# Kernel optimization log

Measured on AMD Instinct MI355X. Metric: run time of the kernel, lower is better.

## Reference

```python
import jax, jax.numpy as jnp
import numpy as np

D_MODEL = 2048
N_HEAD = 16
B, T = 2, 2048
D_HEAD = D_MODEL // N_HEAD          # 128
D_Q = D_MODEL // 3                  # 682
D_KV = D_MODEL // 2                 # 1024
D_QK_N = D_HEAD // 2                # 64
D_QK_R = D_HEAD // 2                # 64
LN_EPS = 1e-5


def setup_inputs() -> dict:
    key = jax.random.key(0)
    ks = jax.random.split(key, 8)
    s = 0.02
    return {
        'x': jax.random.normal(ks[0], (B, T, D_MODEL), dtype=jnp.float32),
        'Wdq_w': jax.random.normal(ks[1], (D_Q, D_MODEL), dtype=jnp.float32) * s,
        'Wdq_b': jnp.zeros((D_Q,), jnp.float32),
        'qn_g': jnp.ones((D_Q,), jnp.float32),
        'qn_b': jnp.zeros((D_Q,), jnp.float32),
        'Wuq_w': jax.random.normal(ks[2], (D_MODEL, D_Q), dtype=jnp.float32) * s,
        'Wuq_b': jnp.zeros((D_MODEL,), jnp.float32),
        'Wdkv_w': jax.random.normal(ks[3], (D_KV + D_QK_R, D_MODEL), dtype=jnp.float32) * s,
        'Wdkv_b': jnp.zeros((D_KV + D_QK_R,), jnp.float32),
        'kvn_g': jnp.ones((D_KV,), jnp.float32),
        'kvn_b': jnp.zeros((D_KV,), jnp.float32),
        'Wukv_w': jax.random.normal(ks[4], (D_MODEL + N_HEAD * D_QK_N, D_KV), dtype=jnp.float32) * s,
        'Wukv_b': jnp.zeros((D_MODEL + N_HEAD * D_QK_N,), jnp.float32),
        'Wo_w': jax.random.normal(ks[5], (D_MODEL, D_MODEL), dtype=jnp.float32) * s,
        'Wo_b': jnp.zeros((D_MODEL,), jnp.float32),
    }


def _linear(x, w, b):
    return jnp.einsum('...i,oi->...o', x, w) + b


def _layernorm(x, g, b):
    mu = jnp.mean(x, axis=-1, keepdims=True)
    var = jnp.mean(jnp.square(x - mu), axis=-1, keepdims=True)
    return (x - mu) * jax.lax.rsqrt(var + LN_EPS) * g + b


def _rotary(x):
    # Faithful to source: positions are taken from axis 1 of x (B, A, T, d)
    A, d = x.shape[1], x.shape[-1]
    inv_freq = (1.0 / 10000.0) ** (jnp.arange(0, d, 2, dtype=jnp.float32) / d)
    freqs = jnp.arange(A, dtype=jnp.float32)[:, None] * inv_freq[None, :]
    cos = jnp.cos(freqs)[None, :, None, :]
    sin = jnp.sin(freqs)[None, :, None, :]
    x1, x2 = jnp.split(x, 2, axis=-1)
    return jnp.concatenate([x1 * cos + x2 * sin, -x1 * sin + x2 * cos], axis=-1)


def reference(x, Wdq_w, Wdq_b, qn_g, qn_b, Wuq_w, Wuq_b,
              Wdkv_w, Wdkv_b, kvn_g, kvn_b, Wukv_w, Wukv_b, Wo_w, Wo_b):
    Bx, Tx, C = x.shape
    # Q path: down-proj -> norm -> up-proj
    c_q = _layernorm(_linear(x, Wdq_w, Wdq_b), qn_g, qn_b)
    q = _linear(c_q, Wuq_w, Wuq_b).reshape(Bx, Tx, N_HEAD, D_HEAD).transpose(0, 2, 1, 3)
    q_n, q_r = q[..., :D_QK_N], q[..., D_QK_N:]
    q_r = _rotary(q_r)
    # KV path
    c_kv = _linear(x, Wdkv_w, Wdkv_b)
    kv_n, k_r = c_kv[..., :D_KV], c_kv[..., D_KV:]
    kv_n = _layernorm(kv_n, kvn_g, kvn_b)
    kv = _linear(kv_n, Wukv_w, Wukv_b).reshape(Bx, Tx, N_HEAD, D_HEAD + D_QK_N).transpose(0, 2, 1, 3)
    k_n, v = kv[..., :D_QK_N], kv[..., D_QK_N:]
    k_r = k_r.reshape(Bx, Tx, 1, D_QK_R).transpose(0, 2, 1, 3)  # (B,1,T,dr)
    k_r = _rotary(k_r)  # identity here (single position), kept for fidelity
    k_r = jnp.broadcast_to(k_r, (Bx, N_HEAD, Tx, D_QK_R))
    q_full = jnp.concatenate([q_n, q_r], axis=-1)   # (B,H,T,d_head)
    k_full = jnp.concatenate([k_n, k_r], axis=-1)   # (B,H,T,d_head)
    # causal SDPA (scale = 1/sqrt(q dim))
    scale = 1.0 / np.sqrt(D_HEAD)
    scores = jnp.einsum('bhqd,bhkd->bhqk', q_full, k_full) * scale
    causal = jnp.tril(jnp.ones((Tx, Tx), dtype=bool))
    scores = jnp.where(causal[None, None], scores, jnp.finfo(scores.dtype).min)
    p = jax.nn.softmax(scores, axis=-1)
    y = jnp.einsum('bhqk,bhkd->bhqd', p, v)
    y = y.transpose(0, 2, 1, 3).reshape(Bx, Tx, C)
    return _linear(y, Wo_w, Wo_b)
```

## Files before the change

kernel.cpp:

```cpp
#include <hip/hip_runtime.h>
#include <math.h>

#define TOK 4096
#define DM 2048
#define DQ 682
#define DQP 704
#define DKV 1024
#define DUKV 3072
#define NH 16
#define T_SEQ 2048
#define NQKV 1792

typedef __attribute__((ext_vector_type(8))) short short8;
typedef __attribute__((ext_vector_type(4))) float floatx4;
typedef __attribute__((ext_vector_type(2))) unsigned int uint2v;

__device__ __forceinline__ unsigned short f2bf(float f) {
  union { float f; unsigned int u; } v; v.f = f;
  unsigned int u = v.u;
  u += 0x7fffu + ((u >> 16) & 1u);
  return (unsigned short)(u >> 16);
}
__device__ __forceinline__ unsigned short f2bf_fast(float f) {
  union { float f; unsigned int u; } v; v.f = f;
  return (unsigned short)((v.u + 0x8000u) >> 16);
}

typedef __attribute__((address_space(1))) const unsigned int as1_u32;
typedef __attribute__((address_space(3))) unsigned int as3_u32;
__device__ __forceinline__ void async16(const void* g, void* l) {
  __builtin_amdgcn_global_load_lds((as1_u32*)g, (as3_u32*)l, 16, 0, 0);
}

__global__ __launch_bounds__(256) void gemm_dqkv_sk(
    const unsigned short* __restrict__ A,
    const unsigned short* __restrict__ B,
    float* __restrict__ P0, float* __restrict__ P1)
{
  __shared__ __align__(16) unsigned short sm[16384];
  const int kz = blockIdx.z;
  const unsigned short* Ab = A + kz * 1024;
  const unsigned short* Bb = B + kz * 1024;
  float* C = kz ? P1 : P0;
  const int K = 1024;

  const int tid = threadIdx.x;
  const int w = tid >> 6, lane = tid & 63, q = lane >> 4, r = lane & 15;
  const int bm = blockIdx.y * 128, bn = blockIdx.x * 128;

  floatx4 acc[4][4];
#pragma unroll
  for (int i = 0; i < 4; i++)
#pragma unroll
    for (int j = 0; j < 4; j++) acc[i][j] = (floatx4){0.f, 0.f, 0.f, 0.f};

  const int srow = tid >> 2, scol = (tid & 3) * 8;
  const unsigned short* Ag0 = Ab + (size_t)(bm + srow) * 2048 + scol;
  const unsigned short* Ag1 = Ab + (size_t)(bm + 64 + srow) * 2048 + scol;
  const unsigned short* Bg0 = Bb + (size_t)(bn + srow) * 2048 + scol;
  const unsigned short* Bg1 = Bb + (size_t)(bn + 64 + srow) * 2048 + scol;
  const int mrow0 = (w >> 1) * 64, ncol0 = (w & 1) * 64;

  async16(Ag0, &sm[w * 512]);
  async16(Ag1, &sm[2048 + w * 512]);
  async16(Bg0, &sm[8192 + w * 512]);
  async16(Bg1, &sm[8192 + 2048 + w * 512]);

  for (int k0 = 0; k0 < K; k0 += 32) {
    const int cur = (k0 >> 5) & 1;
    __syncthreads();
    if (k0 + 32 < K) {
      const int nxt = cur ^ 1;
      async16(Ag0 + k0 + 32, &sm[nxt * 4096 + w * 512]);
      async16(Ag1 + k0 + 32, &sm[nxt * 4096 + 2048 + w * 512]);
      async16(Bg0 + k0 + 32, &sm[8192 + nxt * 4096 + w * 512]);
      async16(Bg1 + k0 + 32, &sm[8192 + nxt * 4096 + 2048 + w * 512]);
    }
    const unsigned short* As = &sm[cur * 4096];
    const unsigned short* Bs = &sm[8192 + cur * 4096];
    short8 a[4], b[4];
#pragma unroll
    for (int i = 0; i < 4; i++)
      a[i] = *(const short8*)&As[(mrow0 + i * 16 + r) * 32 + q * 8];
#pragma unroll
    for (int j = 0; j < 4; j++)
      b[j] = *(const short8*)&Bs[(ncol0 + j * 16 + r) * 32 + q * 8];
#pragma unroll
    for (int i = 0; i < 4; i++)
#pragma unroll
      for (int j = 0; j < 4; j++)
        acc[i][j] = __builtin_amdgcn_mfma_f32_16x16x32_bf16(a[i], b[j], acc[i][j], 0, 0, 0);
  }

#pragma unroll
  for (int j = 0; j < 4; j++) {
    int gc = bn + ncol0 + j * 16 + r;
#pragma unroll
    for (int i = 0; i < 4; i++) {
#pragma unroll
      for (int v = 0; v < 4; v++) {
        int gr = bm + mrow0 + i * 16 + q * 4 + v;
        C[(size_t)gr * NQKV + gc] = acc[i][j][v];
      }
    }
  }
}

__global__ __launch_bounds__(256) void gemm_wo64(
    const unsigned short* __restrict__ A,
    const unsigned short* __restrict__ B,
    const float* __restrict__ bias, float* __restrict__ C)
{
  __shared__ __align__(16) unsigned short sm[32768];
  const int tid = threadIdx.x;
  const int w = tid >> 6, lane = tid & 63, q = lane >> 4, r = lane & 15;
  const int bm = blockIdx.y * 128, bn = blockIdx.x * 128;

  floatx4 acc[4][4];
#pragma unroll
  for (int i = 0; i < 4; i++)
#pragma unroll
    for (int j = 0; j < 4; j++) acc[i][j] = (floatx4){0.f, 0.f, 0.f, 0.f};

  const int srow = tid >> 2, scol = (tid & 3) * 8;
  const unsigned short* Ag0 = A + (size_t)(bm + srow) * 2048 + scol;
  const unsigned short* Ag1 = A + (size_t)(bm + 64 + srow) * 2048 + scol;
  const unsigned short* Bg0 = B + (size_t)(bn + srow) * 2048 + scol;
  const unsigned short* Bg1 = B + (size_t)(bn + 64 + srow) * 2048 + scol;
  const int mrow0 = (w >> 1) * 64, ncol0 = (w & 1) * 64;

#pragma unroll
  for (int c2 = 0; c2 < 2; c2++) {
    async16(Ag0 + c2 * 32, &sm[c2 * 4096 + w * 512]);
    async16(Ag1 + c2 * 32, &sm[c2 * 4096 + 2048 + w * 512]);
    async16(Bg0 + c2 * 32, &sm[16384 + c2 * 4096 + w * 512]);
    async16(Bg1 + c2 * 32, &sm[16384 + c2 * 4096 + 2048 + w * 512]);
  }

  for (int k0 = 0; k0 < 2048; k0 += 64) {
    const int cur = (k0 >> 6) & 1;
    __syncthreads();
    if (k0 + 64 < 2048) {
      const int nxt = cur ^ 1;
#pragma unroll
      for (int c2 = 0; c2 < 2; c2++) {
        async16(Ag0 + k0 + 64 + c2 * 32, &sm[nxt * 8192 + c2 * 4096 + w * 512]);
        async16(Ag1 + k0 + 64 + c2 * 32, &sm[nxt * 8192 + c2 * 4096 + 2048 + w * 512]);
        async16(Bg0 + k0 + 64 + c2 * 32, &sm[16384 + nxt * 8192 + c2 * 4096 + w * 512]);
        async16(Bg1 + k0 + 64 + c2 * 32, &sm[16384 + nxt * 8192 + c2 * 4096 + 2048 + w * 512]);
      }
    }
#pragma unroll
    for (int c2 = 0; c2 < 2; c2++) {
      const unsigned short* As = &sm[cur * 8192 + c2 * 4096];
      const unsigned short* Bs = &sm[16384 + cur * 8192 + c2 * 4096];
      short8 a[4], b[4];
#pragma unroll
      for (int i = 0; i < 4; i++)
        a[i] = *(const short8*)&As[(mrow0 + i * 16 + r) * 32 + q * 8];
#pragma unroll
      for (int j = 0; j < 4; j++)
        b[j] = *(const short8*)&Bs[(ncol0 + j * 16 + r) * 32 + q * 8];
#pragma unroll
      for (int i = 0; i < 4; i++)
#pragma unroll
        for (int j = 0; j < 4; j++)
          acc[i][j] = __builtin_amdgcn_mfma_f32_16x16x32_bf16(a[i], b[j], acc[i][j], 0, 0, 0);
    }
  }

#pragma unroll
  for (int j = 0; j < 4; j++) {
    int gc = bn + ncol0 + j * 16 + r;
    float bv = bias[gc];
#pragma unroll
    for (int i = 0; i < 4; i++) {
#pragma unroll
      for (int v = 0; v < 4; v++) {
        int gr = bm + mrow0 + i * 16 + q * 4 + v;
        C[(size_t)gr * 2048 + gc] = acc[i][j][v] + bv;
      }
    }
  }
}

__global__ __launch_bounds__(256) void gemm_up_fused(
    const unsigned short* __restrict__ Aq, const unsigned short* __restrict__ Bq,
    const float* __restrict__ biasq, unsigned short* __restrict__ Qall,
    const unsigned short* __restrict__ Akv, const unsigned short* __restrict__ Bkv,
    const float* __restrict__ biaskv,
    unsigned short* __restrict__ Kn, unsigned short* __restrict__ Vb)
{
  __shared__ __align__(16) unsigned short sm[16384];
  const int tid = threadIdx.x;
  const int w = tid >> 6, lane = tid & 63, q = lane >> 4, r = lane & 15;
  const int bx = blockIdx.x;
  const bool isQ = bx < 16;
  const int bn = isQ ? bx * 128 : (bx - 16) * 128;
  const int bm = blockIdx.y * 128;
  const int K = isQ ? DQP : DKV;
  const unsigned short* A = isQ ? Aq : Akv;
  const unsigned short* B = isQ ? Bq : Bkv;

  floatx4 acc[4][4];
#pragma unroll
  for (int i = 0; i < 4; i++)
#pragma unroll
    for (int j = 0; j < 4; j++) acc[i][j] = (floatx4){0.f, 0.f, 0.f, 0.f};

  const int srow = tid >> 2, scol = (tid & 3) * 8;
  const unsigned short* Ag0 = A + (size_t)(bm + srow) * K + scol;
  const unsigned short* Ag1 = A + (size_t)(bm + 64 + srow) * K + scol;
  const unsigned short* Bg0 = B + (size_t)(bn + srow) * K + scol;
  const unsigned short* Bg1 = B + (size_t)(bn + 64 + srow) * K + scol;
  const int mrow0 = (w >> 1) * 64, ncol0 = (w & 1) * 64;

  async16(Ag0, &sm[w * 512]);
  async16(Ag1, &sm[2048 + w * 512]);
  async16(Bg0, &sm[8192 + w * 512]);
  async16(Bg1, &sm[8192 + 2048 + w * 512]);

  for (int k0 = 0; k0 < K; k0 += 32) {
    const int cur = (k0 >> 5) & 1;
    __syncthreads();
    if (k0 + 32 < K) {
      const int nxt = cur ^ 1;
      async16(Ag0 + k0 + 32, &sm[nxt * 4096 + w * 512]);
      async16(Ag1 + k0 + 32, &sm[nxt * 4096 + 2048 + w * 512]);
      async16(Bg0 + k0 + 32, &sm[8192 + nxt * 4096 + w * 512]);
      async16(Bg1 + k0 + 32, &sm[8192 + nxt * 4096 + 2048 + w * 512]);
    }
    const unsigned short* As = &sm[cur * 4096];
    const unsigned short* Bs = &sm[8192 + cur * 4096];
    short8 a[4], b[4];
#pragma unroll
    for (int i = 0; i < 4; i++)
      a[i] = *(const short8*)&As[(mrow0 + i * 16 + r) * 32 + q * 8];
#pragma unroll
    for (int j = 0; j < 4; j++)
      b[j] = *(const short8*)&Bs[(ncol0 + j * 16 + r) * 32 + q * 8];
#pragma unroll
    for (int i = 0; i < 4; i++)
#pragma unroll
      for (int j = 0; j < 4; j++)
        acc[i][j] = __builtin_amdgcn_mfma_f32_16x16x32_bf16(a[i], b[j], acc[i][j], 0, 0, 0);
  }

  if (!isQ) {
#pragma unroll
    for (int j = 0; j < 4; j++) {
      int gc = bn + ncol0 + j * 16 + r;
      float bv = biaskv[gc];
      int hh = gc / 192;
      int rel = gc - hh * 192;
#pragma unroll
      for (int i = 0; i < 4; i++) {
#pragma unroll
        for (int v = 0; v < 4; v++) {
          int gr = bm + mrow0 + i * 16 + q * 4 + v;
          int bb = gr >> 11, tt = gr & 2047;
          int bhh = bb * NH + hh;
          int kt = tt >> 6;
          unsigned short val = f2bf(acc[i][j][v] + bv);
          if (rel < 64) {
            Kn[((size_t)(bhh * 32 + kt)) * 4096 + (rel >> 5) * 2048 +
               (tt & 63) * 32 + ((rel & 31) ^ (((tt >> 1) & 3) << 3))] = val;
          } else {
            int d = rel - 64;
            Vb[((size_t)(bhh * 32 + kt)) * 8192 + ((tt >> 5) & 1) * 4096 +
               d * 32 + ((tt & 31) ^ (((d >> 1) & 3) << 3))] = val;
          }
        }
      }
    }
    return;
  }

  const int h = bx;
  const float QS = (float)(0.08838834764831845 * 1.4426950408889634);
  if ((w & 1) == 0) {
#pragma unroll
    for (int j = 0; j < 4; j++) {
      int d = j * 16 + r;
      float bv = biasq[h * 128 + d];
#pragma unroll
      for (int i = 0; i < 4; i++) {
#pragma unroll
        for (int v = 0; v < 4; v++) {
          int gr = bm + mrow0 + i * 16 + q * 4 + v;
          int bb = gr >> 11, t = gr & 2047;
          Qall[(((size_t)(bb * NH + h)) * T_SEQ + t) * 128 + d] =
              f2bf((acc[i][j][v] + bv) * QS);
        }
      }
    }
  } else {
    float cs[2], sn[2], bv1[2], bv2[2];
#pragma unroll
    for (int jp = 0; jp < 2; jp++) {
      int jj = jp * 16 + r;
      float ang = (float)h * exp2f(-(float)jj * (13.287712379549449f / 32.0f));
      cs[jp] = cosf(ang); sn[jp] = sinf(ang);
      bv1[jp] = biasq[h * 128 + 64 + jj];
      bv2[jp] = biasq[h * 128 + 96 + jj];
    }
#pragma unroll
    for (int i = 0; i < 4; i++) {
#pragma unroll
      for (int v = 0; v < 4; v++) {
        int gr = bm + mrow0 + i * 16 + q * 4 + v;
        int bb = gr >> 11, t = gr & 2047;
        unsigned short* Qr = Qall + (((size_t)(bb * NH + h)) * T_SEQ + t) * 128;
#pragma unroll
        for (int jp = 0; jp < 2; jp++) {
          int jj = jp * 16 + r;
          float x1 = acc[i][jp][v] + bv1[jp];
          float x2 = acc[i][jp + 2][v] + bv2[jp];
          Qr[64 + jj] = f2bf((x1 * cs[jp] + x2 * sn[jp]) * QS);
          Qr[96 + jj] = f2bf((x2 * cs[jp] - x1 * sn[jp]) * QS);
        }
      }
    }
  }
}

__device__ __forceinline__ void cvt_region(
    const float* __restrict__ in, unsigned short* __restrict__ out,
    int irows, int icols, int ocols, long idx)
{
  int rr = (int)(idx / ocols);
  int cc = (int)(idx - (long)rr * ocols);
  out[idx] = (rr < irows && cc < icols) ? f2bf(in[(size_t)rr * icols + cc]) : 0;
}

__global__ __launch_bounds__(256) void prep_all(
    const float* __restrict__ x,
    const float* __restrict__ Wdq_w, const float* __restrict__ Wdkv_w,
    const float* __restrict__ Wuq_w, const float* __restrict__ Wukv_w,
    const float* __restrict__ Wo_w,
    const float* __restrict__ Wdq_b, const float* __restrict__ Wdkv_b,
    unsigned short* __restrict__ x_bf,
    unsigned short* __restrict__ Wqkv_bf, unsigned short* __restrict__ Wuq_bf,
    unsigned short* __restrict__ Wukv_bf, unsigned short* __restrict__ Wo_bf,
    float* __restrict__ bias_qkv)
{
  const long bx = blockIdx.x;
  if (bx < 32768) {
    long idx = bx * 256 + threadIdx.x;
    x_bf[idx] = f2bf(x[idx]);
  } else if (bx < 38400) {
    cvt_region(Wdq_w, Wqkv_bf, 682, 2048, 2048, (bx - 32768) * 256 + threadIdx.x);
  } else if (bx < 47104) {
    cvt_region(Wdkv_w, Wqkv_bf + 704L * 2048, 1088, 2048, 2048,
               (bx - 38400) * 256 + threadIdx.x);
  } else if (bx < 52736) {
    cvt_region(Wuq_w, Wuq_bf, 2048, 682, 704, (bx - 47104) * 256 + threadIdx.x);
  } else if (bx < 65024) {
    cvt_region(Wukv_w, Wukv_bf, 3072, 1024, 1024, (bx - 52736) * 256 + threadIdx.x);
  } else if (bx < 81408) {
    cvt_region(Wo_w, Wo_bf, 2048, 2048, 2048, (bx - 65024) * 256 + threadIdx.x);
  } else {
    int i = (int)(bx - 81408) * 256 + threadIdx.x;
    if (i < NQKV)
      bias_qkv[i] = (i < DQ) ? Wdq_b[i] : ((i < DQP) ? 0.f : Wdkv_b[i - DQP]);
  }
}

__global__ __launch_bounds__(256) void ln_dual_r(
    const float* __restrict__ p0, const float* __restrict__ p1,
    const float* __restrict__ bqkv,
    unsigned short* __restrict__ outq, unsigned short* __restrict__ outkv,
    unsigned short* __restrict__ Kr,
    const float* __restrict__ qg, const float* __restrict__ qb2,
    const float* __restrict__ kg, const float* __restrict__ kb2)
{
  __shared__ float sbuf[8];
  const int blk = blockIdx.x;
  if (blk >= 8192) {
    const int base = (blk - 8192) * 512;
#pragma unroll
    for (int s = 0; s < 2; s++) {
      int idx = base + s * 256 + threadIdx.x;
      int row = idx >> 6, dr = idx & 63;
      size_t off = (size_t)row * NQKV + 1728 + dr;
      float v = p0[off] + p1[off] + bqkv[1728 + dr];
      Kr[((size_t)((row >> 11) * 32 + ((row & 2047) >> 6))) * 4096 +
         (dr >> 5) * 2048 + (row & 63) * 32 +
         ((dr & 31) ^ (((row >> 1) & 3) << 3))] = f2bf(v);
    }
    return;
  }
  const bool isQ = blk < 4096;
  const int r2 = isQ ? blk : blk - 4096;
  const int off = isQ ? 0 : DQP;
  const float* x0 = p0 + (size_t)r2 * NQKV + off;
  const float* x1 = p1 + (size_t)r2 * NQKV + off;
  const float* bb = bqkv + off;
  const int D = isQ ? DQ : DKV;
  const int ocols = isQ ? DQP : DKV;
  const float* g = isQ ? qg : kg;
  const float* bta = isQ ? qb2 : kb2;
  unsigned short* orow = (isQ ? outq : outkv) + (size_t)r2 * ocols;

  float s = 0.f, s2 = 0.f;
  float vv[4];
#pragma unroll
  for (int ii = 0; ii < 4; ii++) {
    int i = threadIdx.x + ii * 256;
    if (i < D) {
      float v = x0[i] + x1[i] + bb[i];
      vv[ii] = v;
      s += v; s2 += v * v;
    }
  }
#pragma unroll
  for (int o = 32; o > 0; o >>= 1) {
    s += __shfl_down(s, o, 64);
    s2 += __shfl_down(s2, o, 64);
  }
  int wid = threadIdx.x >> 6;
  __syncthreads();
  if ((threadIdx.x & 63) == 0) { sbuf[wid] = s; sbuf[4 + wid] = s2; }
  __syncthreads();
  float su = sbuf[0] + sbuf[1] + sbuf[2] + sbuf[3];
  float sq = sbuf[4] + sbuf[5] + sbuf[6] + sbuf[7];
  float mu = su / (float)D;
  float var = sq / (float)D - mu * mu;
  float rstd = rsqrtf(var + 1e-5f);
#pragma unroll
  for (int ii = 0; ii < 4; ii++) {
    int i = threadIdx.x + ii * 256;
    if (i < ocols)
      orow[i] = (i < D) ? f2bf((vv[ii] - mu) * rstd * g[i] + bta[i]) : 0;
  }
}

__global__ __launch_bounds__(256, 2) void attn_mfma6(
    const unsigned short* __restrict__ Qall,
    const unsigned short* __restrict__ Kn,
    const unsigned short* __restrict__ Kr,
    const unsigned short* __restrict__ Vb,
    unsigned short* __restrict__ y)
{
  __shared__ __align__(16) unsigned short sm[37376];
  const int id = (int)blockIdx.x;
  const int bhid = id & 31;
  const int pr = id >> 5;
  const int h = bhid & 15, b = bhid >> 4;
  const int tid = threadIdx.x;
  const int w = tid >> 6, lane = tid & 63, q = lane >> 4, r = lane & 15;
  const int bh = bhid;
  const int sq8 = (q ^ ((r >> 1) & 3)) * 8;

  const char* KnG = (const char*)(Kn + (size_t)bh * 32 * 4096);
  const char* KrG = (const char*)(Kr + (size_t)b * 32 * 4096);
  const char* VG  = (const char*)(Vb + (size_t)bh * 32 * 8192);
  char* smB = (char*)sm;
  unsigned short* Psw = sm + 32768 + w * 1152;

#define PREFETCH_KV(kt_, buf_)                                                 \
  {                                                                            \
    const char* kn_ = KnG + (size_t)(kt_) * 8192;                              \
    const char* kr_ = KrG + (size_t)(kt_) * 8192;                              \
    const char* vg_ = VG + (size_t)(kt_) * 16384;                              \
    char* kd_ = smB + (buf_) * 16384;                                          \
    char* vd_ = smB + 32768 + (buf_) * 16384;                                  \
    _Pragma("unroll")                                                          \
    for (int i_ = 0; i_ < 2; i_++) {                                           \
      async16(kn_ + i_ * 4096 + w * 1024 + lane * 16,                          \
              kd_ + i_ * 4096 + w * 1024);                                     \
      async16(kr_ + i_ * 4096 + w * 1024 + lane * 16,                          \
              kd_ + 8192 + i_ * 4096 + w * 1024);                              \
    }                                                                          \
    _Pragma("unroll")                                                          \
    for (int i_ = 0; i_ < 4; i_++)                                             \
      async16(vg_ + i_ * 4096 + w * 1024 + lane * 16,                          \
              vd_ + i_ * 4096 + w * 1024);                                     \
  }

  for (int seg = 0; seg < 2; seg++) {
    const int a = seg ? (31 - pr) : pr;
    if (seg) __syncthreads();
    PREFETCH_KV(0, 0);

    short8 qb[4];
    const unsigned short* Qrow =
        Qall + ((size_t)bh * T_SEQ + (size_t)a * 64 + w * 16 + r) * 128 + q * 8;
#pragma unroll
    for (int c = 0; c < 4; c++) qb[c] = *(const short8*)(Qrow + c * 32);

    floatx4 oacc[8];
#pragma unroll
    for (int jd = 0; jd < 8; jd++) oacc[jd] = (floatx4){0.f, 0.f, 0.f, 0.f};
    float m_i = -3.0e38f, l_i = 0.f;

    for (int kt = 0; kt <= a; kt++) {
      const int cur = kt & 1;
      __syncthreads();
      if (kt < a) PREFETCH_KV(kt + 1, cur ^ 1);

      const unsigned short* KsC = sm + cur * 8192;
      const unsigned short* VsC = sm + 16384 + cur * 8192;

      floatx4 sacc[4];
#pragma unroll
      for (int j = 0; j < 4; j++) sacc[j] = (floatx4){0.f, 0.f, 0.f, 0.f};
      __builtin_amdgcn_s_setprio(1);
#pragma unroll
      for (int c = 0; c < 4; c++) {
        short8 ak[4];
#pragma unroll
        for (int j = 0; j < 4; j++)
          ak[j] = *(const short8*)&KsC[c * 2048 + (j * 16 + r) * 32 + sq8];
#pragma unroll
        for (int j = 0; j < 4; j++)
          sacc[j] = __builtin_amdgcn_mfma_f32_16x16x32_bf16(ak[j], qb[c], sacc[j], 0, 0, 0);
      }
      __builtin_amdgcn_s_setprio(0);

      float sv[16];
#pragma unroll
      for (int j = 0; j < 4; j++)
#pragma unroll
        for (int v = 0; v < 4; v++) sv[j * 4 + v] = sacc[j][v];
      const int rel = (a - kt) * 64 + w * 16 + r;
      if (rel < 63) {
#pragma unroll
        for (int j = 0; j < 4; j++)
#pragma unroll
          for (int v = 0; v < 4; v++)
            if (j * 16 + q * 4 + v > rel) sv[j * 4 + v] = -3.0e38f;
      }
      float tm[8];
#pragma unroll
      for (int t = 0; t < 8; t++) tm[t] = fmaxf(sv[t], sv[t + 8]);
#pragma unroll
      for (int t = 0; t < 4; t++) tm[t] = fmaxf(tm[t], tm[t + 4]);
      float rm = fmaxf(fmaxf(tm[0], tm[2]), fmaxf(tm[1], tm[3]));
      rm = fmaxf(rm, __shfl_xor(rm, 16, 64));
      rm = fmaxf(rm, __shfl_xor(rm, 32, 64));
      if (__any(rm > m_i + 8.f)) {
        float mnew = fmaxf(m_i, rm);
        float alpha = exp2f(m_i - mnew);
        m_i = mnew;
        l_i *= alpha;
#pragma unroll
        for (int jd = 0; jd < 8; jd++) {
          oacc[jd][0] *= alpha; oacc[jd][1] *= alpha;
          oacc[jd][2] *= alpha; oacc[jd][3] *= alpha;
        }
      }
      float p[16];
#pragma unroll
      for (int t = 0; t < 16; t++) p[t] = exp2f(sv[t] - m_i);
      float ts[8];
#pragma unroll
      for (int t = 0; t < 8; t++) ts[t] = p[t] + p[t + 8];
#pragma unroll
      for (int t = 0; t < 4; t++) ts[t] = ts[t] + ts[t + 4];
      float rsum = (ts[0] + ts[2]) + (ts[1] + ts[3]);
      rsum += __shfl_xor(rsum, 16, 64);
      rsum += __shfl_xor(rsum, 32, 64);
      l_i += rsum;
#pragma unroll
      for (int j = 0; j < 4; j++) {
        unsigned int lo = (unsigned int)f2bf_fast(p[j * 4 + 0]) |
                          ((unsigned int)f2bf_fast(p[j * 4 + 1]) << 16);
        unsigned int hi = (unsigned int)f2bf_fast(p[j * 4 + 2]) |
                          ((unsigned int)f2bf_fast(p[j * 4 + 3]) << 16);
        uint2v pk; pk[0] = lo; pk[1] = hi;
        *(uint2v*)&Psw[r * 72 + j * 16 + q * 4] = pk;
      }
      __builtin_amdgcn_s_setprio(1);
#pragma unroll
      for (int c2 = 0; c2 < 2; c2++) {
        short8 pb = *(const short8*)&Psw[r * 72 + c2 * 32 + q * 8];
#pragma unroll
        for (int jd = 0; jd < 8; jd++) {
          short8 bv = *(const short8*)&VsC[c2 * 4096 + (jd * 16 + r) * 32 + sq8];
          oacc[jd] = __builtin_amdgcn_mfma_f32_16x16x32_bf16(bv, pb, oacc[jd], 0, 0, 0);
        }
      }
      __builtin_amdgcn_s_setprio(0);
    }

    float inv = 1.0f / l_i;
    unsigned short* yr =
        y + ((size_t)(b * T_SEQ) + (size_t)a * 64 + w * 16 + r) * DM + h * 128;
#pragma unroll
    for (int jd = 0; jd < 8; jd++) {
      unsigned short o0 = f2bf(oacc[jd][0] * inv);
      unsigned short o1 = f2bf(oacc[jd][1] * inv);
      unsigned short o2 = f2bf(oacc[jd][2] * inv);
      unsigned short o3 = f2bf(oacc[jd][3] * inv);
      unsigned int lo = (unsigned int)o0 | ((unsigned int)o1 << 16);
      unsigned int hi = (unsigned int)o2 | ((unsigned int)o3 << 16);
      unsigned int* dst = (unsigned int*)(yr + jd * 16 + q * 4);
      dst[0] = lo; dst[1] = hi;
    }
  }
#undef PREFETCH_KV
}

extern "C" void kernel_launch(void* const* d_in, const int* in_sizes, int n_in,
                              void* d_out, int out_size, void* d_ws, size_t ws_size,
                              hipStream_t stream) {
  const float* x      = (const float*)d_in[0];
  const float* Wdq_w  = (const float*)d_in[1];
  const float* Wdq_b  = (const float*)d_in[2];
  const float* qn_g   = (const float*)d_in[3];
  const float* qn_b   = (const float*)d_in[4];
  const float* Wuq_w  = (const float*)d_in[5];
  const float* Wuq_b  = (const float*)d_in[6];
  const float* Wdkv_w = (const float*)d_in[7];
  const float* Wdkv_b = (const float*)d_in[8];
  const float* kvn_g  = (const float*)d_in[9];
  const float* kvn_b  = (const float*)d_in[10];
  const float* Wukv_w = (const float*)d_in[11];
  const float* Wukv_b = (const float*)d_in[12];
  const float* Wo_w   = (const float*)d_in[13];
  const float* Wo_b   = (const float*)d_in[14];
  float* out = (float*)d_out;

  float* ws = (float*)d_ws;
  unsigned short* x_bf    = (unsigned short*)(ws);
  unsigned short* y_bf    = (unsigned short*)(ws);
  unsigned short* Wqkv_bf = (unsigned short*)(ws + 4194304);
  unsigned short* Wuq_bf  = (unsigned short*)(ws + 6029312);
  unsigned short* Wukv_bf = (unsigned short*)(ws + 6750208);
  float* bias_qkv = ws + 8323072;
  float* p0       = ws + 8324864;
  float* p1       = ws + 15664896;
  unsigned short* c_q_bf = (unsigned short*)(ws + 23004928);
  unsigned short* kvn_bf = (unsigned short*)(ws + 24446720);
  unsigned short* Q_all  = (unsigned short*)(ws + 26543872);
  unsigned short* Kn_blk = (unsigned short*)(ws + 30738176);
  unsigned short* Kr_blk = (unsigned short*)(ws + 32835328);
  unsigned short* V_blk  = (unsigned short*)(ws + 32966400);
  unsigned short* Wo_bf  = (unsigned short*)(ws + 37160704);

  dim3 blk(256);

  prep_all<<<81415, blk, 0, stream>>>(x, Wdq_w, Wdkv_w, Wuq_w, Wukv_w, Wo_w,
                                      Wdq_b, Wdkv_b,
                                      x_bf, Wqkv_bf, Wuq_bf, Wukv_bf, Wo_bf,
                                      bias_qkv);
  gemm_dqkv_sk<<<dim3(14, 32, 2), blk, 0, stream>>>(x_bf, Wqkv_bf, p0, p1);
  ln_dual_r<<<8704, blk, 0, stream>>>(p0, p1, bias_qkv, c_q_bf, kvn_bf, Kr_blk,
                                      qn_g, qn_b, kvn_g, kvn_b);
  gemm_up_fused<<<dim3(40, 32), blk, 0, stream>>>(c_q_bf, Wuq_bf, Wuq_b, Q_all,
                                                  kvn_bf, Wukv_bf, Wukv_b,
                                                  Kn_blk, V_blk);
  attn_mfma6<<<512, blk, 0, stream>>>(Q_all, Kn_blk, Kr_blk, V_blk, y_bf);
  gemm_wo64<<<dim3(16, 32), blk, 0, stream>>>(y_bf, Wo_bf, Wo_b, out);
}
```

Measured before the change: 396.1 us.

## Split attention KV tile across wave pairs with in-block softmax merge

Doubles the attention block to 512 threads. Each pair of waves shares one 16-row query group, and each wave handles half of every 64-key tile, keeping its own online-softmax state. The two partial outputs are merged through shared memory at the end. The goal is more waves in flight per CU and shorter per-wave serial chains. The cost is an extra LDS round trip and merge, a larger LDS footprint, and idle waves on the diagonal tiles.

```diff
diff --git a/kernel.cpp b/kernel.cpp
--- a/kernel.cpp
+++ b/kernel.cpp
@@ -435,20 +435,21 @@
   }
 }
 
-__global__ __launch_bounds__(256, 2) void attn_mfma6(
+__global__ __launch_bounds__(512, 4) void attn_mfma7(
     const unsigned short* __restrict__ Qall,
     const unsigned short* __restrict__ Kn,
     const unsigned short* __restrict__ Kr,
     const unsigned short* __restrict__ Vb,
     unsigned short* __restrict__ y)
 {
-  __shared__ __align__(16) unsigned short sm[37376];
+  __shared__ __align__(16) unsigned short sm[38144];
   const int id = (int)blockIdx.x;
   const int bhid = id & 31;
   const int pr = id >> 5;
   const int h = bhid & 15, b = bhid >> 4;
   const int tid = threadIdx.x;
   const int w = tid >> 6, lane = tid & 63, q = lane >> 4, r = lane & 15;
+  const int g = w >> 1, hf = w & 1;
   const int bh = bhid;
   const int sq8 = (q ^ ((r >> 1) & 3)) * 8;
 
@@ -456,26 +457,27 @@
   const char* KrG = (const char*)(Kr + (size_t)b * 32 * 4096);
   const char* VG  = (const char*)(Vb + (size_t)bh * 32 * 8192);
   char* smB = (char*)sm;
-  unsigned short* Psw = sm + 32768 + w * 1152;
+  unsigned short* Psw = sm + 32768 + w * 640;
 
 #define PREFETCH_KV(kt_, buf_)                                                 \
   {                                                                            \
-    const char* kn_ = KnG + (size_t)(kt_) * 8192;                              \
-    const char* kr_ = KrG + (size_t)(kt_) * 8192;                              \
-    const char* vg_ = VG + (size_t)(kt_) * 16384;                              \
     char* kd_ = smB + (buf_) * 16384;                                          \
     char* vd_ = smB + 32768 + (buf_) * 16384;                                  \
-    _Pragma("unroll")                                                          \
-    for (int i_ = 0; i_ < 2; i_++) {                                           \
-      async16(kn_ + i_ * 4096 + w * 1024 + lane * 16,                          \
-              kd_ + i_ * 4096 + w * 1024);                                     \
-      async16(kr_ + i_ * 4096 + w * 1024 + lane * 16,                          \
-              kd_ + 8192 + i_ * 4096 + w * 1024);                              \
+    const char* src_;                                                          \
+    char* dst_;                                                                \
+    if (w < 2) {                                                               \
+      src_ = KnG + (size_t)(kt_) * 8192 + w * 4096;                            \
+      dst_ = kd_ + w * 4096;                                                   \
+    } else if (w < 4) {                                                        \
+      src_ = KrG + (size_t)(kt_) * 8192 + (w - 2) * 4096;                      \
+      dst_ = kd_ + 8192 + (w - 2) * 4096;                                      \
+    } else {                                                                   \
+      src_ = VG + (size_t)(kt_) * 16384 + (w - 4) * 4096;                      \
+      dst_ = vd_ + (w - 4) * 4096;                                             \
     }                                                                          \
     _Pragma("unroll")                                                          \
     for (int i_ = 0; i_ < 4; i_++)                                             \
-      async16(vg_ + i_ * 4096 + w * 1024 + lane * 16,                          \
-              vd_ + i_ * 4096 + w * 1024);                                     \
+      async16(src_ + i_ * 1024 + lane * 16, dst_ + i_ * 1024);                 \
   }
 
   for (int seg = 0; seg < 2; seg++) {
@@ -485,7 +487,7 @@
 
     short8 qb[4];
     const unsigned short* Qrow =
-        Qall + ((size_t)bh * T_SEQ + (size_t)a * 64 + w * 16 + r) * 128 + q * 8;
+        Qall + ((size_t)bh * T_SEQ + (size_t)a * 64 + g * 16 + r) * 128 + q * 8;
 #pragma unroll
     for (int c = 0; c < 4; c++) qb[c] = *(const short8*)(Qrow + c * 32);
 
@@ -499,104 +501,125 @@
       __syncthreads();
       if (kt < a) PREFETCH_KV(kt + 1, cur ^ 1);
 
-      const unsigned short* KsC = sm + cur * 8192;
-      const unsigned short* VsC = sm + 16384 + cur * 8192;
-
-      floatx4 sacc[4];
-#pragma unroll
-      for (int j = 0; j < 4; j++) sacc[j] = (floatx4){0.f, 0.f, 0.f, 0.f};
-      __builtin_amdgcn_s_setprio(1);
-#pragma unroll
-      for (int c = 0; c < 4; c++) {
-        short8 ak[4];
-#pragma unroll
-        for (int j = 0; j < 4; j++)
-          ak[j] = *(const short8*)&KsC[c * 2048 + (j * 16 + r) * 32 + sq8];
-#pragma unroll
-        for (int j = 0; j < 4; j++)
-          sacc[j] = __builtin_amdgcn_mfma_f32_16x16x32_bf16(ak[j], qb[c], sacc[j], 0, 0, 0);
-      }
-      __builtin_amdgcn_s_setprio(0);
-
-      float sv[16];
-#pragma unroll
-      for (int j = 0; j < 4; j++)
-#pragma unroll
-        for (int v = 0; v < 4; v++) sv[j * 4 + v] = sacc[j][v];
-      const int rel = (a - kt) * 64 + w * 16 + r;
-      if (rel < 63) {
-#pragma unroll
-        for (int j = 0; j < 4; j++)
-#pragma unroll
-          for (int v = 0; v < 4; v++)
-            if (j * 16 + q * 4 + v > rel) sv[j * 4 + v] = -3.0e38f;
-      }
-      float tm[8];
-#pragma unroll
-      for (int t = 0; t < 8; t++) tm[t] = fmaxf(sv[t], sv[t + 8]);
-#pragma unroll
-      for (int t = 0; t < 4; t++) tm[t] = fmaxf(tm[t], tm[t + 4]);
-      float rm = fmaxf(fmaxf(tm[0], tm[2]), fmaxf(tm[1], tm[3]));
-      rm = fmaxf(rm, __shfl_xor(rm, 16, 64));
-      rm = fmaxf(rm, __shfl_xor(rm, 32, 64));
-      if (__any(rm > m_i + 8.f)) {
-        float mnew = fmaxf(m_i, rm);
-        float alpha = exp2f(m_i - mnew);
-        m_i = mnew;
-        l_i *= alpha;
-#pragma unroll
-        for (int jd = 0; jd < 8; jd++) {
-          oacc[jd][0] *= alpha; oacc[jd][1] *= alpha;
-          oacc[jd][2] *= alpha; oacc[jd][3] *= alpha;
-        }
-      }
-      float p[16];
-#pragma unroll
-      for (int t = 0; t < 16; t++) p[t] = exp2f(sv[t] - m_i);
-      float ts[8];
-#pragma unroll
-      for (int t = 0; t < 8; t++) ts[t] = p[t] + p[t + 8];
-#pragma unroll
-      for (int t = 0; t < 4; t++) ts[t] = ts[t] + ts[t + 4];
-      float rsum = (ts[0] + ts[2]) + (ts[1] + ts[3]);
-      rsum += __shfl_xor(rsum, 16, 64);
-      rsum += __shfl_xor(rsum, 32, 64);
-      l_i += rsum;
-#pragma unroll
-      for (int j = 0; j < 4; j++) {
-        unsigned int lo = (unsigned int)f2bf_fast(p[j * 4 + 0]) |
-                          ((unsigned int)f2bf_fast(p[j * 4 + 1]) << 16);
-        unsigned int hi = (unsigned int)f2bf_fast(p[j * 4 + 2]) |
-                          ((unsigned int)f2bf_fast(p[j * 4 + 3]) << 16);
-        uint2v pk; pk[0] = lo; pk[1] = hi;
-        *(uint2v*)&Psw[r * 72 + j * 16 + q * 4] = pk;
-      }
-      __builtin_amdgcn_s_setprio(1);
-#pragma unroll
-      for (int c2 = 0; c2 < 2; c2++) {
-        short8 pb = *(const short8*)&Psw[r * 72 + c2 * 32 + q * 8];
-#pragma unroll
-        for (int jd = 0; jd < 8; jd++) {
-          short8 bv = *(const short8*)&VsC[c2 * 4096 + (jd * 16 + r) * 32 + sq8];
-          oacc[jd] = __builtin_amdgcn_mfma_f32_16x16x32_bf16(bv, pb, oacc[jd], 0, 0, 0);
-        }
-      }
-      __builtin_amdgcn_s_setprio(0);
-    }
-
-    float inv = 1.0f / l_i;
-    unsigned short* yr =
-        y + ((size_t)(b * T_SEQ) + (size_t)a * 64 + w * 16 + r) * DM + h * 128;
-#pragma unroll
-    for (int jd = 0; jd < 8; jd++) {
-      unsigned short o0 = f2bf(oacc[jd][0] * inv);
-      unsigned short o1 = f2bf(oacc[jd][1] * inv);
-      unsigned short o2 = f2bf(oacc[jd][2] * inv);
-      unsigned short o3 = f2bf(oacc[jd][3] * inv);
-      unsigned int lo = (unsigned int)o0 | ((unsigned int)o1 << 16);
-      unsigned int hi = (unsigned int)o2 | ((unsigned int)o3 << 16);
-      unsigned int* dst = (unsigned int*)(yr + jd * 16 + q * 4);
-      dst[0] = lo; dst[1] = hi;
+      const bool act = ((a - kt) * 64 + g * 16 + 15 - hf * 32) >= 0;
+      if (act) {
+        const unsigned short* KsC = sm + cur * 8192;
+        const unsigned short* VsC = sm + 16384 + cur * 8192 + hf * 4096;
+
+        floatx4 sacc[2];
+        sacc[0] = (floatx4){0.f, 0.f, 0.f, 0.f};
+        sacc[1] = (floatx4){0.f, 0.f, 0.f, 0.f};
+        __builtin_amdgcn_s_setprio(1);
+#pragma unroll
+        for (int c = 0; c < 4; c++) {
+          short8 ak[2];
+#pragma unroll
+          for (int j = 0; j < 2; j++)
+            ak[j] = *(const short8*)&KsC[c * 2048 + ((hf * 2 + j) * 16 + r) * 32 + sq8];
+#pragma unroll
+          for (int j = 0; j < 2; j++)
+            sacc[j] = __builtin_amdgcn_mfma_f32_16x16x32_bf16(ak[j], qb[c], sacc[j], 0, 0, 0);
+        }
+        __builtin_amdgcn_s_setprio(0);
+
+        float sv[8];
+#pragma unroll
+        for (int j = 0; j < 2; j++)
+#pragma unroll
+          for (int v = 0; v < 4; v++) sv[j * 4 + v] = sacc[j][v];
+        const int rel = (a - kt) * 64 + g * 16 + r - hf * 32;
+        if (rel < 31) {
+#pragma unroll
+          for (int j = 0; j < 2; j++)
+#pragma unroll
+            for (int v = 0; v < 4; v++)
+              if (j * 16 + q * 4 + v > rel) sv[j * 4 + v] = -3.0e38f;
+        }
+        float tm[4];
+#pragma unroll
+        for (int t = 0; t < 4; t++) tm[t] = fmaxf(sv[t], sv[t + 4]);
+        float rm = fmaxf(fmaxf(tm[0], tm[1]), fmaxf(tm[2], tm[3]));
+        rm = fmaxf(rm, __shfl_xor(rm, 16, 64));
+        rm = fmaxf(rm, __shfl_xor(rm, 32, 64));
+        if (__any(rm > m_i + 8.f)) {
+          float mnew = fmaxf(m_i, rm);
+          float alpha = exp2f(m_i - mnew);
+          m_i = mnew;
+          l_i *= alpha;
+#pragma unroll
+          for (int jd = 0; jd < 8; jd++) {
+            oacc[jd][0] *= alpha; oacc[jd][1] *= alpha;
+            oacc[jd][2] *= alpha; oacc[jd][3] *= alpha;
+          }
+        }
+        float p[8];
+#pragma unroll
+        for (int t = 0; t < 8; t++) p[t] = exp2f(sv[t] - m_i);
+        float ts[4];
+#pragma unroll
+        for (int t = 0; t < 4; t++) ts[t] = p[t] + p[t + 4];
+        float rsum = (ts[0] + ts[1]) + (ts[2] + ts[3]);
+        rsum += __shfl_xor(rsum, 16, 64);
+        rsum += __shfl_xor(rsum, 32, 64);
+        l_i += rsum;
+#pragma unroll
+        for (int j = 0; j < 2; j++) {
+          unsigned int lo = (unsigned int)f2bf_fast(p[j * 4 + 0]) |
+                            ((unsigned int)f2bf_fast(p[j * 4 + 1]) << 16);
+          unsigned int hi = (unsigned int)f2bf_fast(p[j * 4 + 2]) |
+                            ((unsigned int)f2bf_fast(p[j * 4 + 3]) << 16);
+          uint2v pk; pk[0] = lo; pk[1] = hi;
+          *(uint2v*)&Psw[r * 40 + j * 16 + q * 4] = pk;
+        }
+        __builtin_amdgcn_s_setprio(1);
+        {
+          short8 pb = *(const short8*)&Psw[r * 40 + q * 8];
+#pragma unroll
+          for (int jd = 0; jd < 8; jd++) {
+            short8 bv = *(const short8*)&VsC[(jd * 16 + r) * 32 + sq8];
+            oacc[jd] = __builtin_amdgcn_mfma_f32_16x16x32_bf16(bv, pb, oacc[jd], 0, 0, 0);
+          }
+        }
+        __builtin_amdgcn_s_setprio(0);
+      }
+    }
+
+    __syncthreads();
+    float* mo = (float*)(smB + 32768);
+    float* ml = (float*)(smB + 75776);
+    if (hf) {
+#pragma unroll
+      for (int jd = 0; jd < 8; jd++) {
+        int dsw = (jd * 16 + q * 4) ^ ((r & 7) << 4);
+        *(floatx4*)&mo[g * 2048 + r * 128 + dsw] = oacc[jd];
+      }
+      if (q == 0) {
+        ml[(g * 16 + r) * 2] = m_i;
+        ml[(g * 16 + r) * 2 + 1] = l_i;
+      }
+    }
+    __syncthreads();
+    if (!hf) {
+      float m2 = ml[(g * 16 + r) * 2], l2 = ml[(g * 16 + r) * 2 + 1];
+      float mm = fmaxf(m_i, m2);
+      float s1 = exp2f(m_i - mm), s2 = exp2f(m2 - mm);
+      float linv = 1.0f / (l_i * s1 + l2 * s2);
+      s1 *= linv; s2 *= linv;
+      unsigned short* yr =
+          y + ((size_t)(b * T_SEQ) + (size_t)a * 64 + g * 16 + r) * DM + h * 128;
+#pragma unroll
+      for (int jd = 0; jd < 8; jd++) {
+        int dsw = (jd * 16 + q * 4) ^ ((r & 7) << 4);
+        floatx4 o2 = *(const floatx4*)&mo[g * 2048 + r * 128 + dsw];
+        unsigned short o0 = f2bf(oacc[jd][0] * s1 + o2[0] * s2);
+        unsigned short o1 = f2bf(oacc[jd][1] * s1 + o2[1] * s2);
+        unsigned short o2b = f2bf(oacc[jd][2] * s1 + o2[2] * s2);
+        unsigned short o3 = f2bf(oacc[jd][3] * s1 + o2[3] * s2);
+        unsigned int lo = (unsigned int)o0 | ((unsigned int)o1 << 16);
+        unsigned int hi = (unsigned int)o2b | ((unsigned int)o3 << 16);
+        unsigned int* dst = (unsigned int*)(yr + jd * 16 + q * 4);
+        dst[0] = lo; dst[1] = hi;
+      }
     }
   }
 #undef PREFETCH_KV
@@ -651,6 +674,6 @@
   gemm_up_fused<<<dim3(40, 32), blk, 0, stream>>>(c_q_bf, Wuq_bf, Wuq_b, Q_all,
                                                   kvn_bf, Wukv_bf, Wukv_b,
                                                   Kn_blk, V_blk);
-  attn_mfma6<<<512, blk, 0, stream>>>(Q_all, Kn_blk, Kr_blk, V_blk, y_bf);
+  attn_mfma7<<<512, dim3(512), 0, stream>>>(Q_all, Kn_blk, Kr_blk, V_blk, y_bf);
   gemm_wo64<<<dim3(16, 32), blk, 0, stream>>>(y_bf, Wo_bf, Wo_b, out);
 }
```

Measured after the change: 403.6 us. Within noise of the previous version (+1.9%).

## Process 128-row query tiles per block with two 16-row groups per wave

Applied to the files above, without the earlier changes.

Reorganizes the attention kernel so each block handles one 128-row query tile, with each wave computing two 16-row groups. This replaces the earlier scheme of two paired 64-row tiles per block. Each K/V tile staged in shared memory and each V fragment read from LDS is reused across twice as many query rows, cutting LDS and global traffic per FLOP. The cost is higher register pressure from doubled accumulators, and the causal load balance per block is now uneven and depends on launch ordering.

```diff
diff --git a/kernel.cpp b/kernel.cpp
--- a/kernel.cpp
+++ b/kernel.cpp
@@ -435,7 +435,7 @@
   }
 }
 
-__global__ __launch_bounds__(256, 2) void attn_mfma6(
+__global__ __launch_bounds__(256, 2) void attn_mfma8(
     const unsigned short* __restrict__ Qall,
     const unsigned short* __restrict__ Kn,
     const unsigned short* __restrict__ Kr,
@@ -445,7 +445,8 @@
   __shared__ __align__(16) unsigned short sm[37376];
   const int id = (int)blockIdx.x;
   const int bhid = id & 31;
-  const int pr = id >> 5;
+  const int idx = (id >> 5) & 7;
+  const int qt = (id >= 256) ? (15 - idx) : idx;
   const int h = bhid & 15, b = bhid >> 4;
   const int tid = threadIdx.x;
   const int w = tid >> 6, lane = tid & 63, q = lane >> 4, r = lane & 15;
@@ -457,6 +458,7 @@
   const char* VG  = (const char*)(Vb + (size_t)bh * 32 * 8192);
   char* smB = (char*)sm;
   unsigned short* Psw = sm + 32768 + w * 1152;
+  const int ktmax = 2 * qt + 1;
 
 #define PREFETCH_KV(kt_, buf_)                                                 \
   {                                                                            \
@@ -478,33 +480,39 @@
               vd_ + i_ * 4096 + w * 1024);                                     \
   }
 
-  for (int seg = 0; seg < 2; seg++) {
-    const int a = seg ? (31 - pr) : pr;
-    if (seg) __syncthreads();
-    PREFETCH_KV(0, 0);
-
-    short8 qb[4];
+  PREFETCH_KV(0, 0);
+
+  short8 qb[2][4];
+#pragma unroll
+  for (int g = 0; g < 2; g++) {
     const unsigned short* Qrow =
-        Qall + ((size_t)bh * T_SEQ + (size_t)a * 64 + w * 16 + r) * 128 + q * 8;
-#pragma unroll
-    for (int c = 0; c < 4; c++) qb[c] = *(const short8*)(Qrow + c * 32);
-
-    floatx4 oacc[8];
-#pragma unroll
-    for (int jd = 0; jd < 8; jd++) oacc[jd] = (floatx4){0.f, 0.f, 0.f, 0.f};
-    float m_i = -3.0e38f, l_i = 0.f;
-
-    for (int kt = 0; kt <= a; kt++) {
-      const int cur = kt & 1;
-      __syncthreads();
-      if (kt < a) PREFETCH_KV(kt + 1, cur ^ 1);
-
+        Qall + ((size_t)bh * T_SEQ + (size_t)qt * 128 + w * 32 + g * 16 + r) * 128 + q * 8;
+#pragma unroll
+    for (int c = 0; c < 4; c++) qb[g][c] = *(const short8*)(Qrow + c * 32);
+  }
+
+  floatx4 oacc[2][8];
+#pragma unroll
+  for (int g = 0; g < 2; g++)
+#pragma unroll
+    for (int jd = 0; jd < 8; jd++) oacc[g][jd] = (floatx4){0.f, 0.f, 0.f, 0.f};
+  float m_i[2] = {-3.0e38f, -3.0e38f}, l_i[2] = {0.f, 0.f};
+
+  for (int kt = 0; kt <= ktmax; kt++) {
+    const int cur = kt & 1;
+    __syncthreads();
+    if (kt < ktmax) PREFETCH_KV(kt + 1, cur ^ 1);
+
+    const bool activeW = (kt * 64 <= qt * 128 + w * 32 + 31);
+    if (activeW) {
       const unsigned short* KsC = sm + cur * 8192;
       const unsigned short* VsC = sm + 16384 + cur * 8192;
 
-      floatx4 sacc[4];
-#pragma unroll
-      for (int j = 0; j < 4; j++) sacc[j] = (floatx4){0.f, 0.f, 0.f, 0.f};
+      floatx4 sacc[2][4];
+#pragma unroll
+      for (int g = 0; g < 2; g++)
+#pragma unroll
+        for (int j = 0; j < 4; j++) sacc[g][j] = (floatx4){0.f, 0.f, 0.f, 0.f};
       __builtin_amdgcn_s_setprio(1);
 #pragma unroll
       for (int c = 0; c < 4; c++) {
@@ -513,86 +521,98 @@
         for (int j = 0; j < 4; j++)
           ak[j] = *(const short8*)&KsC[c * 2048 + (j * 16 + r) * 32 + sq8];
 #pragma unroll
+        for (int g = 0; g < 2; g++)
+#pragma unroll
+          for (int j = 0; j < 4; j++)
+            sacc[g][j] = __builtin_amdgcn_mfma_f32_16x16x32_bf16(ak[j], qb[g][c], sacc[g][j], 0, 0, 0);
+      }
+      __builtin_amdgcn_s_setprio(0);
+
+      short8 pb[2][2];
+#pragma unroll
+      for (int g = 0; g < 2; g++) {
+        float sv[16];
+#pragma unroll
         for (int j = 0; j < 4; j++)
-          sacc[j] = __builtin_amdgcn_mfma_f32_16x16x32_bf16(ak[j], qb[c], sacc[j], 0, 0, 0);
-      }
-      __builtin_amdgcn_s_setprio(0);
-
-      float sv[16];
-#pragma unroll
-      for (int j = 0; j < 4; j++)
-#pragma unroll
-        for (int v = 0; v < 4; v++) sv[j * 4 + v] = sacc[j][v];
-      const int rel = (a - kt) * 64 + w * 16 + r;
-      if (rel < 63) {
-#pragma unroll
-        for (int j = 0; j < 4; j++)
-#pragma unroll
-          for (int v = 0; v < 4; v++)
-            if (j * 16 + q * 4 + v > rel) sv[j * 4 + v] = -3.0e38f;
-      }
-      float tm[8];
-#pragma unroll
-      for (int t = 0; t < 8; t++) tm[t] = fmaxf(sv[t], sv[t + 8]);
-#pragma unroll
-      for (int t = 0; t < 4; t++) tm[t] = fmaxf(tm[t], tm[t + 4]);
-      float rm = fmaxf(fmaxf(tm[0], tm[2]), fmaxf(tm[1], tm[3]));
-      rm = fmaxf(rm, __shfl_xor(rm, 16, 64));
-      rm = fmaxf(rm, __shfl_xor(rm, 32, 64));
-      if (__any(rm > m_i + 8.f)) {
-        float mnew = fmaxf(m_i, rm);
-        float alpha = exp2f(m_i - mnew);
-        m_i = mnew;
-        l_i *= alpha;
-#pragma unroll
-        for (int jd = 0; jd < 8; jd++) {
-          oacc[jd][0] *= alpha; oacc[jd][1] *= alpha;
-          oacc[jd][2] *= alpha; oacc[jd][3] *= alpha;
+#pragma unroll
+          for (int v = 0; v < 4; v++) sv[j * 4 + v] = sacc[g][j][v];
+        const int rel = qt * 128 + w * 32 + g * 16 + r - kt * 64;
+        if (rel < 63) {
+#pragma unroll
+          for (int j = 0; j < 4; j++)
+#pragma unroll
+            for (int v = 0; v < 4; v++)
+              if (j * 16 + q * 4 + v > rel) sv[j * 4 + v] = -3.0e38f;
         }
-      }
-      float p[16];
-#pragma unroll
-      for (int t = 0; t < 16; t++) p[t] = exp2f(sv[t] - m_i);
-      float ts[8];
-#pragma unroll
-      for (int t = 0; t < 8; t++) ts[t] = p[t] + p[t + 8];
-#pragma unroll
-      for (int t = 0; t < 4; t++) ts[t] = ts[t] + ts[t + 4];
-      float rsum = (ts[0] + ts[2]) + (ts[1] + ts[3]);
-      rsum += __shfl_xor(rsum, 16, 64);
-      rsum += __shfl_xor(rsum, 32, 64);
-      l_i += rsum;
-#pragma unroll
-      for (int j = 0; j < 4; j++) {
-        unsigned int lo = (unsigned int)f2bf_fast(p[j * 4 + 0]) |
-                          ((unsigned int)f2bf_fast(p[j * 4 + 1]) << 16);
-        unsigned int hi = (unsigned int)f2bf_fast(p[j * 4 + 2]) |
-                          ((unsigned int)f2bf_fast(p[j * 4 + 3]) << 16);
-        uint2v pk; pk[0] = lo; pk[1] = hi;
-        *(uint2v*)&Psw[r * 72 + j * 16 + q * 4] = pk;
-      }
+        float tm[8];
+#pragma unroll
+        for (int t = 0; t < 8; t++) tm[t] = fmaxf(sv[t], sv[t + 8]);
+#pragma unroll
+        for (int t = 0; t < 4; t++) tm[t] = fmaxf(tm[t], tm[t + 4]);
+        float rm = fmaxf(fmaxf(tm[0], tm[2]), fmaxf(tm[1], tm[3]));
+        rm = fmaxf(rm, __shfl_xor(rm, 16, 64));
+        rm = fmaxf(rm, __shfl_xor(rm, 32, 64));
+        if (__any(rm > m_i[g] + 8.f)) {
+          float mnew = fmaxf(m_i[g], rm);
+          float alpha = exp2f(m_i[g] - mnew);
+          m_i[g] = mnew;
+          l_i[g] *= alpha;
+#pragma unroll
+          for (int jd = 0; jd < 8; jd++) {
+            oacc[g][jd][0] *= alpha; oacc[g][jd][1] *= alpha;
+            oacc[g][jd][2] *= alpha; oacc[g][jd][3] *= alpha;
+          }
+        }
+        float p[16];
+#pragma unroll
+        for (int t = 0; t < 16; t++) p[t] = exp2f(sv[t] - m_i[g]);
+        float ts[8];
+#pragma unroll
+        for (int t = 0; t < 8; t++) ts[t] = p[t] + p[t + 8];
+#pragma unroll
+        for (int t = 0; t < 4; t++) ts[t] = ts[t] + ts[t + 4];
+        float rsum = (ts[0] + ts[2]) + (ts[1] + ts[3]);
+        rsum += __shfl_xor(rsum, 16, 64);
+        rsum += __shfl_xor(rsum, 32, 64);
+        l_i[g] += rsum;
+#pragma unroll
+        for (int j = 0; j < 4; j++) {
+          unsigned int lo = (unsigned int)f2bf_fast(p[j * 4 + 0]) |
+                            ((unsigned int)f2bf_fast(p[j * 4 + 1]) << 16);
+          unsigned int hi = (unsigned int)f2bf_fast(p[j * 4 + 2]) |
+                            ((unsigned int)f2bf_fast(p[j * 4 + 3]) << 16);
+          uint2v pk; pk[0] = lo; pk[1] = hi;
+          *(uint2v*)&Psw[r * 72 + j * 16 + q * 4] = pk;
+        }
+        pb[g][0] = *(const short8*)&Psw[r * 72 + q * 8];
+        pb[g][1] = *(const short8*)&Psw[r * 72 + 32 + q * 8];
+      }
+
       __builtin_amdgcn_s_setprio(1);
 #pragma unroll
       for (int c2 = 0; c2 < 2; c2++) {
-        short8 pb = *(const short8*)&Psw[r * 72 + c2 * 32 + q * 8];
 #pragma unroll
         for (int jd = 0; jd < 8; jd++) {
           short8 bv = *(const short8*)&VsC[c2 * 4096 + (jd * 16 + r) * 32 + sq8];
-          oacc[jd] = __builtin_amdgcn_mfma_f32_16x16x32_bf16(bv, pb, oacc[jd], 0, 0, 0);
+          oacc[0][jd] = __builtin_amdgcn_mfma_f32_16x16x32_bf16(bv, pb[0][c2], oacc[0][jd], 0, 0, 0);
+          oacc[1][jd] = __builtin_amdgcn_mfma_f32_16x16x32_bf16(bv, pb[1][c2], oacc[1][jd], 0, 0, 0);
         }
       }
       __builtin_amdgcn_s_setprio(0);
     }
-
-    float inv = 1.0f / l_i;
+  }
+
+#pragma unroll
+  for (int g = 0; g < 2; g++) {
+    float inv = 1.0f / l_i[g];
     unsigned short* yr =
-        y + ((size_t)(b * T_SEQ) + (size_t)a * 64 + w * 16 + r) * DM + h * 128;
+        y + ((size_t)(b * T_SEQ) + (size_t)qt * 128 + w * 32 + g * 16 + r) * DM + h * 128;
 #pragma unroll
     for (int jd = 0; jd < 8; jd++) {
-      unsigned short o0 = f2bf(oacc[jd][0] * inv);
-      unsigned short o1 = f2bf(oacc[jd][1] * inv);
-      unsigned short o2 = f2bf(oacc[jd][2] * inv);
-      unsigned short o3 = f2bf(oacc[jd][3] * inv);
+      unsigned short o0 = f2bf(oacc[g][jd][0] * inv);
+      unsigned short o1 = f2bf(oacc[g][jd][1] * inv);
+      unsigned short o2 = f2bf(oacc[g][jd][2] * inv);
+      unsigned short o3 = f2bf(oacc[g][jd][3] * inv);
       unsigned int lo = (unsigned int)o0 | ((unsigned int)o1 << 16);
       unsigned int hi = (unsigned int)o2 | ((unsigned int)o3 << 16);
       unsigned int* dst = (unsigned int*)(yr + jd * 16 + q * 4);
@@ -651,6 +671,6 @@
   gemm_up_fused<<<dim3(40, 32), blk, 0, stream>>>(c_q_bf, Wuq_bf, Wuq_b, Q_all,
                                                   kvn_bf, Wukv_bf, Wukv_b,
                                                   Kn_blk, V_blk);
-  attn_mfma6<<<512, blk, 0, stream>>>(Q_all, Kn_blk, Kr_blk, V_blk, y_bf);
+  attn_mfma8<<<512, blk, 0, stream>>>(Q_all, Kn_blk, Kr_blk, V_blk, y_bf);
   gemm_wo64<<<dim3(16, 32), blk, 0, stream>>>(y_bf, Wo_bf, Wo_b, out);
 }
```

Measured after the change: 406.1 us. +2.5%, slower.
